# Kernel tuning notes

Hardware: AMD Instinct MI355X
Metric: run time of the kernel (lower is better)

The kernel has to match this reference:

```python
import jax, jax.numpy as jnp
import numpy as np
import math

N = 8192
F_IN = 1024
F_OUT = 1024
MAX_ITER = 10


def whale_optimizer(positions, key, max_iter=MAX_ITER):
    """Vectorized whale optimization algorithm.

    Faithful to the original per-agent/per-dim update rules, but the agent
    loop is vectorized (on-device RNG, one parallel update per outer
    iteration); only the `max_iter` outer iterations stay sequential.
    positions: [N, D] float32.
    """
    n, d = positions.shape
    lower = jnp.min(positions)
    upper = jnp.max(positions)
    k0, loop_key = jax.random.split(key)
    leader = positions[jax.random.randint(k0, (), 0, n)]  # [D]

    def step(carry, it):
        pos, leader = carry
        itf = it.astype(jnp.float32)
        k = jax.random.fold_in(loop_key, it)
        k1, k2, k3, k4, k5, k6 = jax.random.split(k, 6)
        a = 2.0 - itf * (2.0 / max_iter)
        a2 = -1.0 + itf * (-1.0 / max_iter)
        r1 = jax.random.uniform(k1, (n, 1))
        r2 = jax.random.uniform(k2, (n, 1))
        A = 2.0 * a * r1 - a                       # [n,1]
        C = 2.0 * r2                               # [n,1]
        lp = (a2 - 1.0) * jax.random.uniform(k3, (n, 1)) + 1.0  # spiral param
        p = jax.random.uniform(k4, (n, 1))
        # random leader per (agent, dim), as in the original inner j-loop
        ridx = jax.random.randint(k5, (n, d), 0, n)
        x_rand = jnp.take_along_axis(pos, ridx, axis=0)         # [n,d]
        explore = jnp.abs(x_rand - A * jnp.abs(C * x_rand - pos))
        exploit = jnp.abs(leader - A * jnp.abs(C * leader - pos))
        spiral = jnp.abs(jnp.abs(leader - pos) * jnp.exp(lp) * jnp.cos(2.0 * jnp.pi * lp) + leader)
        new_pos = jnp.where(p < 0.5,
                            jnp.where(jnp.abs(A) >= 1.0, explore, exploit),
                            spiral)
        new_pos = jnp.clip(new_pos, lower, upper)
        new_leader = new_pos[jax.random.randint(k6, (), 0, n)]
        return (new_pos, new_leader), None

    (positions, _), _ = jax.lax.scan(step, (positions, leader), jnp.arange(max_iter))
    return positions


def setup_inputs() -> dict:
    key = jax.random.key(0)
    k1, k2, k3, k4 = jax.random.split(key, 4)
    stdv = 1.0 / math.sqrt(F_OUT)
    return {
        "input": jax.random.normal(k1, (N, F_IN), dtype=jnp.float32),
        "adj": jax.random.uniform(k2, (N, N), dtype=jnp.float32) * (1.0 / N),
        "h0": jax.random.normal(k3, (N, F_IN), dtype=jnp.float32),
        "weight": jax.random.uniform(k4, (F_IN, F_OUT), dtype=jnp.float32,
                                      minval=-stdv, maxval=stdv),
        "lamda": jnp.float32(0.5),
        "alpha": jnp.float32(0.1),
        "l": 1,
    }


def reference(input, adj, h0, weight, lamda, alpha, l):
    # variant=False, residual=False
    theta = jnp.log(lamda / l + 1.0)
    hi = adj @ input                                  # spmm(adj, input)
    support = (1.0 - alpha) * hi + alpha * h0
    r = support
    # original detaches support before the whale optimizer
    opt = whale_optimizer(jax.lax.stop_gradient(support), jax.random.key(42))
    output = theta * (opt @ weight) + (1.0 - theta) * r
    return output
```

## Files before the change

### kernel.cpp

```cpp
#include <hip/hip_runtime.h>
#include <hip/hip_bf16.h>
#include <stdint.h>
#include <math.h>

typedef uint32_t u32;
typedef __hip_bfloat16 bf16t;
typedef __attribute__((ext_vector_type(8))) short short8;
typedef __attribute__((ext_vector_type(4))) float f32x4;


__host__ __device__ __forceinline__ void tf2(u32 k0, u32 k1, u32 c0, u32 c1, u32& o0, u32& o1) {
  const u32 ks2 = k0 ^ k1 ^ 0x1BD11BDAu;
  u32 x0 = c0 + k0, x1 = c1 + k1;
#define TFROT(v,r) (((v)<<(r))|((v)>>(32-(r))))
#define TFR(r) { x0 += x1; x1 = TFROT(x1,r); x1 ^= x0; }
  TFR(13) TFR(15) TFR(26) TFR(6)   x0 += k1;  x1 += ks2 + 1u;
  TFR(17) TFR(29) TFR(16) TFR(24)  x0 += ks2; x1 += k0 + 2u;
  TFR(13) TFR(15) TFR(26) TFR(6)   x0 += k0;  x1 += k1 + 3u;
  TFR(17) TFR(29) TFR(16) TFR(24)  x0 += k1;  x1 += ks2 + 4u;
  TFR(13) TFR(15) TFR(26) TFR(6)   x0 += ks2; x1 += k0 + 5u;
#undef TFR
#undef TFROT
  o0 = x0; o1 = x1;
}

__device__ __forceinline__ float unif_row(u32 ka, u32 kb, int i) {
  u32 o0, o1;
  tf2(ka, kb, 0u, (u32)i, o0, o1);
  return __uint_as_float(0x3F800000u | ((o0 ^ o1) >> 9)) - 1.0f;
}

__device__ __forceinline__ int ridx_fn(u32 ka, u32 kb, u32 f) {
  u32 o0, o1; tf2(ka, kb, 0u, f, o0, o1); return (int)((o0 ^ o1) & 8191u);
}

static inline void split2(u32 ka, u32 kb, u32* kA, u32* kB) {
  u32 a0, a1, b0, b1;
  tf2(ka, kb, 0u, 0u, a0, a1);
  tf2(ka, kb, 0u, 1u, b0, b1);
  kA[0] = a0; kA[1] = a1; kB[0] = b0; kB[1] = b1;
}

static inline void split6(u32 ka, u32 kb, u32 out[6][2]) {
  for (u32 i = 0; i < 6; i++) { u32 o0, o1; tf2(ka, kb, 0u, i, o0, o1); out[i][0] = o0; out[i][1] = o1; }
}

static inline int scalar_randint8192(u32 ka, u32 kb) {
  u32 kA[2], kB[2];
  split2(ka, kb, kA, kB);
  u32 o0, o1;
  tf2(kB[0], kB[1], 0u, 0u, o0, o1);
  return (int)((o0 ^ o1) & 8191u);
}

__device__ __forceinline__ ushort f2bf(float f) {
  u32 u = __float_as_uint(f);
  u32 r = u + 0x7FFFu + ((u >> 16) & 1u);
  return (ushort)(r >> 16);
}

__global__ __launch_bounds__(256) void packb_k(const float* __restrict__ B, uint4* __restrict__ out, int K, int Nn) {
  const int idx = blockIdx.x * 256 + threadIdx.x;
  const int total = (K >> 3) * Nn;
  if (idx >= total) return;
  const int g = idx / Nn;
  const int n = idx - g * Nn;
  u32 wv[4];
#pragma unroll
  for (int j = 0; j < 4; j++) {
    const float f0 = B[(size_t)(g * 8 + 2 * j) * Nn + n];
    const float f1 = B[(size_t)(g * 8 + 2 * j + 1) * Nn + n];
    wv[j] = (u32)f2bf(f0) | ((u32)f2bf(f1) << 16);
  }
  uint4 o; o.x = wv[0]; o.y = wv[1]; o.z = wv[2]; o.w = wv[3];
  out[idx] = o;
}

__global__ __launch_bounds__(256) void packa_k(const float* __restrict__ A, uint4* __restrict__ out,
                                               int M, int K, int lgS) {
  const int idx = blockIdx.x * 256 + threadIdx.x;
  const int S = K >> 6;
  const int total = ((M >> 7) * S) << 10;
  if (idx >= total) return;
  const int chunk = idx >> 10;
  const int w = idx & 1023;
  const int r = w >> 3, kq = w & 7;
  const int cm = chunk >> lgS, s = chunk & (S - 1);
  const float* src = A + (size_t)((cm << 7) + r) * K + (s << 6) + (kq << 3);
  const float4 f0 = *(const float4*)src;
  const float4 f1 = *(const float4*)(src + 4);
  u32 wv[4];
  wv[0] = (u32)f2bf(f0.x) | ((u32)f2bf(f0.y) << 16);
  wv[1] = (u32)f2bf(f0.z) | ((u32)f2bf(f0.w) << 16);
  wv[2] = (u32)f2bf(f1.x) | ((u32)f2bf(f1.y) << 16);
  wv[3] = (u32)f2bf(f1.z) | ((u32)f2bf(f1.w) << 16);
  uint4 o; o.x = wv[0]; o.y = wv[1]; o.z = wv[2]; o.w = wv[3];
  out[((size_t)chunk << 10) + (r << 3) + (kq ^ (r & 7))] = o;
}

__global__ __launch_bounds__(256) void minmax2_k(const float* __restrict__ part, int G, float* __restrict__ bnd) {
  __shared__ float slo[256], shi[256];
  const int tid = threadIdx.x;
  float lo = 3.4e38f, hi = -3.4e38f;
  for (int i = tid; i < G; i += 256) { lo = fminf(lo, part[i]); hi = fmaxf(hi, part[G + i]); }
  slo[tid] = lo; shi[tid] = hi; __syncthreads();
  for (int s = 128; s > 0; s >>= 1) {
    if (tid < s) { slo[tid] = fminf(slo[tid], slo[tid + s]); shi[tid] = fmaxf(shi[tid], shi[tid + s]); }
    __syncthreads();
  }
  if (tid == 0) { bnd[0] = slo[0]; bnd[1] = shi[0]; }
}

__device__ __forceinline__ void gld_lds16(const void* g, void* l) {
  __builtin_amdgcn_global_load_lds((const __attribute__((address_space(1))) void*)g,
                                   (__attribute__((address_space(3))) void*)l, 16, 0, 0);
}

template <int EPI>
__global__ __launch_bounds__(256, 2) void gemm_k(
    const bf16t* __restrict__ Ap, const bf16t* __restrict__ Bp,
    const float* __restrict__ aux, const float* __restrict__ sF,
    const int* __restrict__ sI, float* __restrict__ C,
    float* __restrict__ prt, int PG, int Nn, int K) {
  __shared__ __align__(16) bf16t As[2][8192];
  __shared__ __align__(16) bf16t Bs[2][8192];
  const int tid = threadIdx.x;
  const int lane = tid & 63;
  const int wave = tid >> 6;
  const int bm = blockIdx.x & 63;
  const int bn = blockIdx.x >> 6;
  const int m0 = bm << 7, n0 = bn << 7;
  const int wm = (wave & 1) << 6;
  const int wn = (wave >> 1) << 6;
  const int S = K >> 6;

  f32x4 acc[4][4];
#pragma unroll
  for (int i = 0; i < 4; i++)
#pragma unroll
    for (int j = 0; j < 4; j++) acc[i][j] = (f32x4){0.f, 0.f, 0.f, 0.f};

  const bf16t* gA0 = Ap + (((size_t)bm * S) << 13);
  const bf16t* gBj[4];
  const size_t bstep = (size_t)Nn * 64;
#pragma unroll
  for (int j = 0; j < 4; j++) {
    const int u = tid + (j << 8);
    gBj[j] = Bp + ((size_t)(u >> 7) * Nn + n0 + (u & 127)) * 8;
  }
  auto stage = [&](int s, int buf) {
    const bf16t* a = gA0 + ((size_t)s << 13);
#pragma unroll
    for (int j = 0; j < 4; j++) {
      const int u = tid + (j << 8);
      gld_lds16(a + ((size_t)u << 3), &As[buf][u << 3]);
    }
#pragma unroll
    for (int j = 0; j < 4; j++) {
      const int u = tid + (j << 8);
      gld_lds16(gBj[j] + (size_t)s * bstep, &Bs[buf][u << 3]);
    }
  };

  const int arow = lane & 15, aq = lane >> 4;
  const int abase = ((wm + arow) << 6) + ((aq ^ (arow & 7)) << 3);
  const int bbase = ((aq << 7) + wn + arow) << 3;

  stage(0, 0);

  for (int s = 0; s < S; ++s) {
    const int cur = s & 1;
    __syncthreads();
    if (s + 1 < S) stage(s + 1, cur ^ 1);
#pragma unroll
    for (int c = 0; c < 2; ++c) {
      short8 af[4], bv[4];
      const int ab = abase ^ (c << 5);
#pragma unroll
      for (int mt = 0; mt < 4; mt++)
        af[mt] = *(const short8*)(&As[cur][ab + mt * 1024]);
#pragma unroll
      for (int nt = 0; nt < 4; nt++)
        bv[nt] = *(const short8*)(&Bs[cur][bbase + (c << 12) + (nt << 7)]);
#pragma unroll
      for (int mt = 0; mt < 4; mt++)
#pragma unroll
        for (int nt = 0; nt < 4; nt++)
          acc[mt][nt] = __builtin_amdgcn_mfma_f32_16x16x32_bf16(af[mt], bv[nt], acc[mt][nt], 0, 0, 0);
    }
  }

  float p1, p2;
  if (EPI == 1) { const float al = sF[0]; p1 = 1.0f - al; p2 = al; }
  else { const float th = logf(sF[0] / (float)sI[0] + 1.0f); p1 = th; p2 = 1.0f - th; }
  const int col = lane & 15, rq = lane >> 4;
  float vlo = 3.4e38f, vhi = -3.4e38f;
#pragma unroll
  for (int mt = 0; mt < 4; mt++)
#pragma unroll
    for (int nt = 0; nt < 4; nt++)
#pragma unroll
      for (int r = 0; r < 4; r++) {
        const int gm = m0 + wm + mt * 16 + (rq << 2) + r;
        const int gn = n0 + wn + nt * 16 + col;
        const size_t ix = (size_t)gm * Nn + gn;
        const float v = p1 * acc[mt][nt][r] + p2 * aux[ix];
        C[ix] = v;
        if (EPI == 1) { vlo = fminf(vlo, v); vhi = fmaxf(vhi, v); }
      }
  if (EPI == 1) {
    __syncthreads();
    float* red = (float*)&As[0][0];
    red[tid] = vlo; red[256 + tid] = vhi;
    __syncthreads();
    for (int s = 128; s > 0; s >>= 1) {
      if (tid < s) {
        red[tid] = fminf(red[tid], red[tid + s]);
        red[256 + tid] = fmaxf(red[256 + tid], red[256 + tid + s]);
      }
      __syncthreads();
    }
    if (tid == 0) { prt[blockIdx.x] = red[0]; prt[PG + blockIdx.x] = red[256]; }
  }
}

struct WA {
  u32 k1a, k1b, k2a, k2b, k3a, k3b, k4a, k4b, k5a, k5b;
  int ldr;
  float a, a2;
};

__global__ __launch_bounds__(256) void whale_k(
    const float* __restrict__ pinb, float* __restrict__ poutb,
    ushort* __restrict__ opt, const float* __restrict__ bnd, WA w) {
  const int row = blockIdx.x;
  const int tid = threadIdx.x;
  __shared__ float sh[4];
  if (tid < 4) {
    u32 ka, kb;
    if (tid == 0)      { ka = w.k1a; kb = w.k1b; }
    else if (tid == 1) { ka = w.k2a; kb = w.k2b; }
    else if (tid == 2) { ka = w.k3a; kb = w.k3b; }
    else               { ka = w.k4a; kb = w.k4b; }
    sh[tid] = unif_row(ka, kb, row);
  }
  __syncthreads();
  const float r1 = sh[0], r2 = sh[1], u3 = sh[2], p = sh[3];
  float t2 = (2.0f * w.a) * r1;
  asm volatile("" : "+v"(t2));
  const float A = t2 - w.a;
  const float Cc = 2.0f * r2;
  const float lo = bnd[0], hi = bnd[1];
  const float* pin = pinb + ((size_t)row << 10);
  const int j0 = tid << 2;
  float4 pv = *(const float4*)(pin + j0);
  float ov[4];
  const bool bp = (p < 0.5f);
  if (bp && (fabsf(A) >= 1.0f)) {
    const u32 fb = ((u32)row << 10) + (u32)j0;
#pragma unroll
    for (int e = 0; e < 4; e++) {
      const float pos = (&pv.x)[e];
      const int ri = ridx_fn(w.k5a, w.k5b, fb + (u32)e);
      const float xr = pinb[((size_t)ri << 10) + j0 + e];
      ov[e] = fabsf(xr - A * fabsf(Cc * xr - pos));
    }
  } else {
    const float* ldp = pinb + ((size_t)w.ldr << 10);
    float4 lv = *(const float4*)(ldp + j0);
    if (bp) {
#pragma unroll
      for (int e = 0; e < 4; e++) {
        const float pos = (&pv.x)[e], ld = (&lv.x)[e];
        ov[e] = fabsf(ld - A * fabsf(Cc * ld - pos));
      }
    } else {
      const float lp = (w.a2 - 1.0f) * u3 + 1.0f;
      const float s1 = expf(lp);
      const float s2 = cosf(6.2831855f * lp);
#pragma unroll
      for (int e = 0; e < 4; e++) {
        const float pos = (&pv.x)[e], ld = (&lv.x)[e];
        ov[e] = fabsf(fabsf(ld - pos) * s1 * s2 + ld);
      }
    }
  }
  float4 res;
#pragma unroll
  for (int e = 0; e < 4; e++) (&res.x)[e] = fminf(fmaxf(ov[e], lo), hi);
  *(float4*)(poutb + ((size_t)row << 10) + j0) = res;
  if (opt) {
    ushort4 o4;
    o4.x = f2bf(res.x); o4.y = f2bf(res.y); o4.z = f2bf(res.z); o4.w = f2bf(res.w);
    const int rr = row & 127;
    const size_t chunk = (size_t)((row >> 7) << 4) + (j0 >> 6);
    ushort* dst = opt + (chunk << 13) + (rr << 6) + ((((j0 >> 3) & 7) ^ (rr & 7)) << 3) + (j0 & 7);
    *(ushort4*)dst = o4;
  }
}

extern "C" void kernel_launch(void* const* d_in, const int* in_sizes, int n_in,
                              void* d_out, int out_size, void* d_ws, size_t ws_size,
                              hipStream_t stream) {
  const float* inp = (const float*)d_in[0];
  const float* adj = (const float*)d_in[1];
  const float* h0  = (const float*)d_in[2];
  const float* wgt = (const float*)d_in[3];
  const float* lam = (const float*)d_in[4];
  const float* alp = (const float*)d_in[5];
  const int* lint  = (const int*)d_in[6];

  float* outp = (float*)d_out;

  char* ws = (char*)d_ws;
  bf16t* Apk  = (bf16t*)(ws);
  float* P0   = (float*)(ws);
  float* P1   = (float*)(ws + 33554432);
  ushort* OPT = (ushort*)(ws + 67108864);
  bf16t* B1p  = (bf16t*)(ws + 134217728);
  bf16t* Wp   = (bf16t*)(ws + 150994944);
  float* SUP  = (float*)(ws + 153092096);
  float* PRT  = (float*)(ws + 186646528);
  float* BND  = (float*)(ws + 186662912);

  hipLaunchKernelGGL(packa_k, dim3(32768), dim3(256), 0, stream, adj, (uint4*)Apk, 8192, 8192, 7);
  hipLaunchKernelGGL(packb_k, dim3(4096), dim3(256), 0, stream, inp, (uint4*)B1p, 8192, 1024);
  hipLaunchKernelGGL(packb_k, dim3(512), dim3(256), 0, stream, wgt, (uint4*)Wp, 1024, 1024);
  hipLaunchKernelGGL((gemm_k<1>), dim3(512), dim3(256), 0, stream, Apk, B1p, h0, alp, lint,
                     SUP, PRT, 512, 1024, 8192);
  hipLaunchKernelGGL(minmax2_k, dim3(1), dim3(256), 0, stream, PRT, 512, BND);

  u32 k0k[2], lpk[2];
  split2(0u, 42u, k0k, lpk);
  int ldr = scalar_randint8192(k0k[0], k0k[1]);
  const float* cur = SUP;
  float* bufs[2] = {P0, P1};
  for (int it = 0; it < 10; ++it) {
    u32 ka, kb; tf2(lpk[0], lpk[1], 0u, (u32)it, ka, kb);
    u32 ks[6][2];
    split6(ka, kb, ks);
    u32 k5A[2], k5B[2];
    split2(ks[4][0], ks[4][1], k5A, k5B);
    WA w;
    w.k1a = ks[0][0]; w.k1b = ks[0][1];
    w.k2a = ks[1][0]; w.k2b = ks[1][1];
    w.k3a = ks[2][0]; w.k3b = ks[2][1];
    w.k4a = ks[3][0]; w.k4b = ks[3][1];
    w.k5a = k5B[0];   w.k5b = k5B[1];
    w.ldr = ldr;
    const float itf = (float)it;
    w.a = 2.0f - itf * 0.2f;
    w.a2 = -1.0f + itf * (-0.1f);
    float* nxt = bufs[it & 1];
    hipLaunchKernelGGL(whale_k, dim3(8192), dim3(256), 0, stream, cur, nxt,
                       (it == 9) ? OPT : (ushort*)nullptr, BND, w);
    cur = nxt;
    ldr = scalar_randint8192(ks[5][0], ks[5][1]);
  }
  hipLaunchKernelGGL((gemm_k<2>), dim3(512), dim3(256), 0, stream, (const bf16t*)OPT, Wp, SUP, lam, lint,
                     outp, (float*)nullptr, 0, 1024, 1024);
  (void)in_sizes; (void)n_in; (void)out_size; (void)ws_size;
}
```

Measured before the change: 856.6 us.

## Fuse whale iterations into one cooperative kernel and merge pack launches

Replaces the ten per-iteration whale launches with one cooperative kernel of 1024 blocks. Each wave handles two rows, and a grid.sync separates the iterations. The minmax reduction is folded into every block's prologue, and the three pack kernels are merged into one launch. This removes launch overhead and the inter-kernel gaps, but it drops the fp32 write of the last iteration. It also relies on all 1024 blocks being co-resident and adds grid-barrier cost.

```diff
diff --git a/kernel.cpp b/kernel.cpp
--- a/kernel.cpp
+++ b/kernel.cpp
@@ -1,7 +1,10 @@
 #include <hip/hip_runtime.h>
+#include <hip/hip_cooperative_groups.h>
 #include <hip/hip_bf16.h>
 #include <stdint.h>
 #include <math.h>
+
+namespace cg = cooperative_groups;
 
 typedef uint32_t u32;
 typedef __hip_bfloat16 bf16t;
@@ -59,29 +62,9 @@
   return (ushort)(r >> 16);
 }
 
-__global__ __launch_bounds__(256) void packb_k(const float* __restrict__ B, uint4* __restrict__ out, int K, int Nn) {
-  const int idx = blockIdx.x * 256 + threadIdx.x;
-  const int total = (K >> 3) * Nn;
-  if (idx >= total) return;
-  const int g = idx / Nn;
-  const int n = idx - g * Nn;
-  u32 wv[4];
-#pragma unroll
-  for (int j = 0; j < 4; j++) {
-    const float f0 = B[(size_t)(g * 8 + 2 * j) * Nn + n];
-    const float f1 = B[(size_t)(g * 8 + 2 * j + 1) * Nn + n];
-    wv[j] = (u32)f2bf(f0) | ((u32)f2bf(f1) << 16);
-  }
-  uint4 o; o.x = wv[0]; o.y = wv[1]; o.z = wv[2]; o.w = wv[3];
-  out[idx] = o;
-}
-
-__global__ __launch_bounds__(256) void packa_k(const float* __restrict__ A, uint4* __restrict__ out,
-                                               int M, int K, int lgS) {
-  const int idx = blockIdx.x * 256 + threadIdx.x;
+__device__ __forceinline__ void packa_body(int idx, const float* __restrict__ A, uint4* __restrict__ out,
+                                           int K, int lgS) {
   const int S = K >> 6;
-  const int total = ((M >> 7) * S) << 10;
-  if (idx >= total) return;
   const int chunk = idx >> 10;
   const int w = idx & 1023;
   const int r = w >> 3, kq = w & 7;
@@ -98,17 +81,34 @@
   out[((size_t)chunk << 10) + (r << 3) + (kq ^ (r & 7))] = o;
 }
 
-__global__ __launch_bounds__(256) void minmax2_k(const float* __restrict__ part, int G, float* __restrict__ bnd) {
-  __shared__ float slo[256], shi[256];
+__device__ __forceinline__ void packb_body(int idx, const float* __restrict__ B, uint4* __restrict__ out,
+                                           int Nn) {
+  const int g = idx / Nn;
+  const int n = idx - g * Nn;
+  u32 wv[4];
+#pragma unroll
+  for (int j = 0; j < 4; j++) {
+    const float f0 = B[(size_t)(g * 8 + 2 * j) * Nn + n];
+    const float f1 = B[(size_t)(g * 8 + 2 * j + 1) * Nn + n];
+    wv[j] = (u32)f2bf(f0) | ((u32)f2bf(f1) << 16);
+  }
+  uint4 o; o.x = wv[0]; o.y = wv[1]; o.z = wv[2]; o.w = wv[3];
+  out[idx] = o;
+}
+
+__global__ __launch_bounds__(256) void pack_all_k(
+    const float* __restrict__ adj, uint4* __restrict__ apk,
+    const float* __restrict__ inp, uint4* __restrict__ b1p,
+    const float* __restrict__ wgt, uint4* __restrict__ wp) {
+  const int b = blockIdx.x;
   const int tid = threadIdx.x;
-  float lo = 3.4e38f, hi = -3.4e38f;
-  for (int i = tid; i < G; i += 256) { lo = fminf(lo, part[i]); hi = fmaxf(hi, part[G + i]); }
-  slo[tid] = lo; shi[tid] = hi; __syncthreads();
-  for (int s = 128; s > 0; s >>= 1) {
-    if (tid < s) { slo[tid] = fminf(slo[tid], slo[tid + s]); shi[tid] = fmaxf(shi[tid], shi[tid + s]); }
-    __syncthreads();
-  }
-  if (tid == 0) { bnd[0] = slo[0]; bnd[1] = shi[0]; }
+  if (b < 32768) {
+    packa_body(b * 256 + tid, adj, apk, 8192, 7);
+  } else if (b < 36864) {
+    packb_body((b - 32768) * 256 + tid, inp, b1p, 1024);
+  } else {
+    packb_body((b - 36864) * 256 + tid, wgt, wp, 1024);
+  }
 }
 
 __device__ __forceinline__ void gld_lds16(const void* g, void* l) {
@@ -229,73 +229,100 @@
   int ldr;
   float a, a2;
 };
-
-__global__ __launch_bounds__(256) void whale_k(
-    const float* __restrict__ pinb, float* __restrict__ poutb,
-    ushort* __restrict__ opt, const float* __restrict__ bnd, WA w) {
-  const int row = blockIdx.x;
+struct WAll { WA w[10]; };
+
+__global__ __launch_bounds__(256, 4) void whale_all_k(
+    const float* __restrict__ sup, float* __restrict__ p0, float* __restrict__ p1,
+    ushort* __restrict__ opt, const float* __restrict__ prt, WAll wall) {
+  __shared__ float slo[256], shi[256];
   const int tid = threadIdx.x;
-  __shared__ float sh[4];
-  if (tid < 4) {
-    u32 ka, kb;
-    if (tid == 0)      { ka = w.k1a; kb = w.k1b; }
-    else if (tid == 1) { ka = w.k2a; kb = w.k2b; }
-    else if (tid == 2) { ka = w.k3a; kb = w.k3b; }
-    else               { ka = w.k4a; kb = w.k4b; }
-    sh[tid] = unif_row(ka, kb, row);
-  }
-  __syncthreads();
-  const float r1 = sh[0], r2 = sh[1], u3 = sh[2], p = sh[3];
-  float t2 = (2.0f * w.a) * r1;
-  asm volatile("" : "+v"(t2));
-  const float A = t2 - w.a;
-  const float Cc = 2.0f * r2;
-  const float lo = bnd[0], hi = bnd[1];
-  const float* pin = pinb + ((size_t)row << 10);
-  const int j0 = tid << 2;
-  float4 pv = *(const float4*)(pin + j0);
-  float ov[4];
-  const bool bp = (p < 0.5f);
-  if (bp && (fabsf(A) >= 1.0f)) {
-    const u32 fb = ((u32)row << 10) + (u32)j0;
-#pragma unroll
-    for (int e = 0; e < 4; e++) {
-      const float pos = (&pv.x)[e];
-      const int ri = ridx_fn(w.k5a, w.k5b, fb + (u32)e);
-      const float xr = pinb[((size_t)ri << 10) + j0 + e];
-      ov[e] = fabsf(xr - A * fabsf(Cc * xr - pos));
-    }
-  } else {
-    const float* ldp = pinb + ((size_t)w.ldr << 10);
-    float4 lv = *(const float4*)(ldp + j0);
-    if (bp) {
-#pragma unroll
-      for (int e = 0; e < 4; e++) {
-        const float pos = (&pv.x)[e], ld = (&lv.x)[e];
-        ov[e] = fabsf(ld - A * fabsf(Cc * ld - pos));
+  {
+    float l = fminf(prt[tid], prt[tid + 256]);
+    float h = fmaxf(prt[512 + tid], prt[768 + tid]);
+    slo[tid] = l; shi[tid] = h; __syncthreads();
+    for (int s = 128; s > 0; s >>= 1) {
+      if (tid < s) { slo[tid] = fminf(slo[tid], slo[tid + s]); shi[tid] = fmaxf(shi[tid], shi[tid + s]); }
+      __syncthreads();
+    }
+  }
+  const float lo = slo[0], hi = shi[0];
+
+  cg::grid_group grid = cg::this_grid();
+  const int wave = tid >> 6, lane = tid & 63;
+  const int rbase = blockIdx.x * 8 + wave * 2;
+  const float* cur = sup;
+  for (int it = 0; it < 10; ++it) {
+    float* nxt = (it & 1) ? p1 : p0;
+    const WA w = wall.w[it];
+    const float* ldp = cur + ((size_t)w.ldr << 10);
+#pragma unroll
+    for (int rr = 0; rr < 2; ++rr) {
+      const int row = rbase + rr;
+      const float r1 = unif_row(w.k1a, w.k1b, row);
+      const float r2 = unif_row(w.k2a, w.k2b, row);
+      const float u3 = unif_row(w.k3a, w.k3b, row);
+      const float p  = unif_row(w.k4a, w.k4b, row);
+      float t2 = (2.0f * w.a) * r1;
+      asm volatile("" : "+v"(t2));
+      const float A = t2 - w.a;
+      const float Cc = 2.0f * r2;
+      const float* pin = cur + ((size_t)row << 10);
+      float* pout = nxt + ((size_t)row << 10);
+      const bool bp = (p < 0.5f);
+      const bool ex = bp && (fabsf(A) >= 1.0f);
+      float s1 = 0.f, s2 = 0.f;
+      if (!bp) {
+        const float lp = (w.a2 - 1.0f) * u3 + 1.0f;
+        s1 = expf(lp);
+        s2 = cosf(6.2831855f * lp);
       }
-    } else {
-      const float lp = (w.a2 - 1.0f) * u3 + 1.0f;
-      const float s1 = expf(lp);
-      const float s2 = cosf(6.2831855f * lp);
-#pragma unroll
-      for (int e = 0; e < 4; e++) {
-        const float pos = (&pv.x)[e], ld = (&lv.x)[e];
-        ov[e] = fabsf(fabsf(ld - pos) * s1 * s2 + ld);
+#pragma unroll
+      for (int k = 0; k < 4; ++k) {
+        const int j0 = (lane + (k << 6)) << 2;
+        float4 pv = *(const float4*)(pin + j0);
+        float ov[4];
+        if (ex) {
+          const u32 fb = ((u32)row << 10) + (u32)j0;
+#pragma unroll
+          for (int e = 0; e < 4; ++e) {
+            const float pos = (&pv.x)[e];
+            const int ri = ridx_fn(w.k5a, w.k5b, fb + (u32)e);
+            const float xr = cur[((size_t)ri << 10) + j0 + e];
+            ov[e] = fabsf(xr - A * fabsf(Cc * xr - pos));
+          }
+        } else {
+          float4 lv = *(const float4*)(ldp + j0);
+          if (bp) {
+#pragma unroll
+            for (int e = 0; e < 4; ++e) {
+              const float pos = (&pv.x)[e], ld = (&lv.x)[e];
+              ov[e] = fabsf(ld - A * fabsf(Cc * ld - pos));
+            }
+          } else {
+#pragma unroll
+            for (int e = 0; e < 4; ++e) {
+              const float pos = (&pv.x)[e], ld = (&lv.x)[e];
+              ov[e] = fabsf(fabsf(ld - pos) * s1 * s2 + ld);
+            }
+          }
+        }
+        float4 res;
+#pragma unroll
+        for (int e = 0; e < 4; ++e) (&res.x)[e] = fminf(fmaxf(ov[e], lo), hi);
+        if (it != 9) {
+          *(float4*)(pout + j0) = res;
+        } else {
+          ushort4 o4;
+          o4.x = f2bf(res.x); o4.y = f2bf(res.y); o4.z = f2bf(res.z); o4.w = f2bf(res.w);
+          const int rw = row & 127;
+          const size_t chunk = (size_t)((row >> 7) << 4) + (j0 >> 6);
+          ushort* dst = opt + (chunk << 13) + (rw << 6) + ((((j0 >> 3) & 7) ^ (rw & 7)) << 3) + (j0 & 7);
+          *(ushort4*)dst = o4;
+        }
       }
     }
-  }
-  float4 res;
-#pragma unroll
-  for (int e = 0; e < 4; e++) (&res.x)[e] = fminf(fmaxf(ov[e], lo), hi);
-  *(float4*)(poutb + ((size_t)row << 10) + j0) = res;
-  if (opt) {
-    ushort4 o4;
-    o4.x = f2bf(res.x); o4.y = f2bf(res.y); o4.z = f2bf(res.z); o4.w = f2bf(res.w);
-    const int rr = row & 127;
-    const size_t chunk = (size_t)((row >> 7) << 4) + (j0 >> 6);
-    ushort* dst = opt + (chunk << 13) + (rr << 6) + ((((j0 >> 3) & 7) ^ (rr & 7)) << 3) + (j0 & 7);
-    *(ushort4*)dst = o4;
+    if (it < 9) grid.sync();
+    cur = nxt;
   }
 }
 
@@ -321,27 +348,23 @@
   bf16t* Wp   = (bf16t*)(ws + 150994944);
   float* SUP  = (float*)(ws + 153092096);
   float* PRT  = (float*)(ws + 186646528);
-  float* BND  = (float*)(ws + 186662912);
-
-  hipLaunchKernelGGL(packa_k, dim3(32768), dim3(256), 0, stream, adj, (uint4*)Apk, 8192, 8192, 7);
-  hipLaunchKernelGGL(packb_k, dim3(4096), dim3(256), 0, stream, inp, (uint4*)B1p, 8192, 1024);
-  hipLaunchKernelGGL(packb_k, dim3(512), dim3(256), 0, stream, wgt, (uint4*)Wp, 1024, 1024);
+
+  hipLaunchKernelGGL(pack_all_k, dim3(37376), dim3(256), 0, stream,
+                     adj, (uint4*)Apk, inp, (uint4*)B1p, wgt, (uint4*)Wp);
   hipLaunchKernelGGL((gemm_k<1>), dim3(512), dim3(256), 0, stream, Apk, B1p, h0, alp, lint,
                      SUP, PRT, 512, 1024, 8192);
-  hipLaunchKernelGGL(minmax2_k, dim3(1), dim3(256), 0, stream, PRT, 512, BND);
 
   u32 k0k[2], lpk[2];
   split2(0u, 42u, k0k, lpk);
   int ldr = scalar_randint8192(k0k[0], k0k[1]);
-  const float* cur = SUP;
-  float* bufs[2] = {P0, P1};
+  WAll wall;
   for (int it = 0; it < 10; ++it) {
     u32 ka, kb; tf2(lpk[0], lpk[1], 0u, (u32)it, ka, kb);
     u32 ks[6][2];
     split6(ka, kb, ks);
     u32 k5A[2], k5B[2];
     split2(ks[4][0], ks[4][1], k5A, k5B);
-    WA w;
+    WA& w = wall.w[it];
     w.k1a = ks[0][0]; w.k1b = ks[0][1];
     w.k2a = ks[1][0]; w.k2b = ks[1][1];
     w.k3a = ks[2][0]; w.k3b = ks[2][1];
@@ -351,12 +374,15 @@
     const float itf = (float)it;
     w.a = 2.0f - itf * 0.2f;
     w.a2 = -1.0f + itf * (-0.1f);
-    float* nxt = bufs[it & 1];
-    hipLaunchKernelGGL(whale_k, dim3(8192), dim3(256), 0, stream, cur, nxt,
-                       (it == 9) ? OPT : (ushort*)nullptr, BND, w);
-    cur = nxt;
     ldr = scalar_randint8192(ks[5][0], ks[5][1]);
   }
+  {
+    const float* a0 = SUP; float* a1 = P0; float* a2 = P1; ushort* a3 = OPT;
+    const float* a4 = PRT;
+    void* wargs[] = {(void*)&a0, (void*)&a1, (void*)&a2, (void*)&a3, (void*)&a4, (void*)&wall};
+    hipLaunchCooperativeKernel(whale_all_k, dim3(1024), dim3(256), wargs, 0, stream);
+  }
+
   hipLaunchKernelGGL((gemm_k<2>), dim3(512), dim3(256), 0, stream, (const bf16t*)OPT, Wp, SUP, lam, lint,
                      outp, (float*)nullptr, 0, 1024, 1024);
   (void)in_sizes; (void)n_in; (void)out_size; (void)ws_size;
```

Result: slower. 2.024 ms (+136.3%).
